# Kernel optimization log

Measured on AMD Instinct MI355X. Metric: run time of the kernel, lower is better.

## Reference

```python
import jax, jax.numpy as jnp
import numpy as np


def setup_inputs() -> dict:
    key = jax.random.key(0)
    k1, k2, k3, k4 = jax.random.split(key, 4)
    batch, T, state_dim, action_dim = 64, 1024, 512, 128
    x0 = jax.random.normal(k1, (batch, state_dim), dtype=jnp.float32)
    us = jax.random.normal(k2, (batch, T, action_dim), dtype=jnp.float32)
    # Scale A so the 1024-step linear recurrence stays bounded (spectral radius < 1)
    A = jax.random.normal(k3, (state_dim, state_dim), dtype=jnp.float32) * (0.9 / np.sqrt(state_dim))
    B = jax.random.normal(k4, (action_dim, state_dim), dtype=jnp.float32) * (1.0 / np.sqrt(action_dim))
    return {"x0": x0, "us": us, "A": A, "B": B}


def reference(x0, us, A, B):
    """Linear SSM rollout: x_{t+1} = x_t @ A + u_t @ B, returns xs [batch, T, state_dim]."""
    us_t = jnp.swapaxes(us, 0, 1)  # [T, batch, action_dim]

    def step(x, u):
        x_next = x @ A + u @ B  # [batch, state_dim]
        return x_next, x_next

    _, xs = jax.lax.scan(step, x0, us_t)  # xs: [T, batch, state_dim]
    return jnp.swapaxes(xs, 0, 1)  # [batch, T, state_dim]
```

## Files before the change

kernel.cpp:

```cpp
#include <hip/hip_runtime.h>


typedef __attribute__((ext_vector_type(8))) short bf16x8;
typedef __attribute__((ext_vector_type(8))) unsigned short ushort8;
typedef __attribute__((ext_vector_type(4))) float f32x4;
typedef unsigned short ushort_t;

#define MFMA16(a, b, c) __builtin_amdgcn_mfma_f32_16x16x32_bf16(a, b, c, 0, 0, 0)

#define OFF_AT  0UL
#define OFF_AU  8912896UL
#define OFF_BT  15204352UL
#define OFF_BU  15335424UL
#define OFF_WT  15466496UL
#define OFF_Z   16515072UL
#define OFF_E1S 41680896UL
#define OFF_E2S 50069504UL

__host__ __device__ __forceinline__ int slot_of(int p) {
    if (p == 0) return 16;
    if (p <= 8) return p - 1;
    return 7 + (p >> 3);
}

__device__ __forceinline__ unsigned short f2bf(float f) {
    union { float f; unsigned u; } v; v.f = f;
    unsigned r = v.u + 0x7FFFu + ((v.u >> 16) & 1u);
    return (unsigned short)(r >> 16);
}

__device__ __forceinline__ int sel4(int4 v, int p) {
    return p == 0 ? v.x : p == 1 ? v.y : p == 2 ? v.z : v.w;
}

typedef __attribute__((address_space(3))) unsigned int as3_u32;
typedef __attribute__((address_space(1))) const unsigned int as1_u32;
__device__ __forceinline__ void gll16(const void* g, void* l) {
    __builtin_amdgcn_global_load_lds((as1_u32*)g, (as3_u32*)l, 16, 0, 0);
}

__global__ __launch_bounds__(256) void prep_kernel(const float* __restrict__ A,
                                                   char* __restrict__ ws) {
    ushort_t* At1 = (ushort_t*)(ws + OFF_AT);
    ushort_t* Au1 = (ushort_t*)(ws + OFF_AU);
    long idx = (long)blockIdx.x * 256 + threadIdx.x;
    if (idx < 262144) {
        Au1[idx] = f2bf(A[idx]);
    } else {
        long gi = idx - 262144;
        int n = (int)(gi >> 9), k = (int)(gi & 511);
        At1[gi] = f2bf(A[(long)k * 512 + n]);
    }
}

__device__ __forceinline__ void pow_tile(char* __restrict__ ws, ushort_t* ldsX,
                                         int d, int m_, int i_, int prod,
                                         int mb, int nb) {
    ushort_t* At = (ushort_t*)(ws + OFF_AT);
    ushort_t* Au = (ushort_t*)(ws + OFF_AU);
    const ushort_t *Xp, *Yp; ushort_t* outp;
    if (prod == 0) { Xp = At + (long)slot_of(m_) * 262144; Yp = Au + (long)slot_of(i_) * 262144; outp = At + (long)slot_of(d) * 262144; }
    else           { Xp = Au + (long)slot_of(i_) * 262144; Yp = At + (long)slot_of(m_) * 262144; outp = Au + (long)slot_of(d) * 262144; }

    int tid = threadIdx.x, w = tid >> 6, lane = tid & 63, q = lane >> 4, r = lane & 15;

    for (int i2 = tid; i2 < 64 * 64; i2 += 256) {
        int row = i2 >> 6, c8 = i2 & 63;
        ushort8 v = *(const ushort8*)(Xp + (long)(mb * 64 + row) * 512 + c8 * 8);
        *(ushort8*)&ldsX[row * 512 + ((c8 ^ (row & 7)) << 3)] = v;
    }
    __syncthreads();

    f32x4 acc[4][2];
    for (int a1 = 0; a1 < 4; a1++) for (int b1 = 0; b1 < 2; b1++) acc[a1][b1] = (f32x4){0.f, 0.f, 0.f, 0.f};

    int n0 = nb * 128 + w * 32;
    for (int kt = 0; kt < 16; kt++) {
        bf16x8 b0 = *(const bf16x8*)(Yp + (long)(n0 + r) * 512 + kt * 32 + q * 8);
        bf16x8 b1 = *(const bf16x8*)(Yp + (long)(n0 + 16 + r) * 512 + kt * 32 + q * 8);
        int g2 = kt * 4 + q;
#pragma unroll
        for (int mi = 0; mi < 4; mi++) {
            int row = mi * 16 + r;
            bf16x8 a = *(bf16x8*)&ldsX[row * 512 + ((g2 ^ (row & 7)) << 3)];
            acc[mi][0] = MFMA16(a, b0, acc[mi][0]);
            acc[mi][1] = MFMA16(a, b1, acc[mi][1]);
        }
    }
    for (int mi = 0; mi < 4; mi++) for (int nj = 0; nj < 2; nj++) {
        int m = mb * 64 + mi * 16 + q * 4, n = n0 + nj * 16 + r;
        for (int v = 0; v < 4; v++) outp[(long)(m + v) * 512 + n] = f2bf(acc[mi][nj][v]);
    }
}

__device__ __forceinline__ void wk_tile(char* __restrict__ ws, ushort_t* ldsX,
                                        int k8, int mb) {
    ushort_t* At = (ushort_t*)(ws + OFF_AT);
    ushort_t* Bu = (ushort_t*)(ws + OFF_BU);
    ushort_t* Bt = (ushort_t*)(ws + OFF_BT);
    ushort_t* Wt = (ushort_t*)(ws + OFF_WT);

    int tid = threadIdx.x, w = tid >> 6, lane = tid & 63, q = lane >> 4, r = lane & 15;

    if (k8 == 7) {
        for (int i2 = tid; i2 < 64 * 32; i2 += 256) {
            int row = i2 >> 5, c4 = i2 & 31;
            ushort4 v = *(const ushort4*)(Bt + (long)(mb * 64 + row) * 128 + c4 * 4);
            *(ushort4*)(Wt + (long)(mb * 64 + row) * 128 + c4 * 4) = v;
        }
        return;
    }

    int p = 7 - k8;
    const ushort_t* Xp = At + (long)slot_of(p) * 262144;
    for (int i2 = tid; i2 < 64 * 64; i2 += 256) {
        int row = i2 >> 6, c8 = i2 & 63;
        ushort8 v = *(const ushort8*)(Xp + (long)(mb * 64 + row) * 512 + c8 * 8);
        *(ushort8*)&ldsX[row * 512 + ((c8 ^ (row & 7)) << 3)] = v;
    }
    __syncthreads();

    f32x4 acc[4][2];
    for (int a1 = 0; a1 < 4; a1++) for (int b1 = 0; b1 < 2; b1++) acc[a1][b1] = (f32x4){0.f, 0.f, 0.f, 0.f};

    int n0 = w * 32;
    for (int kt = 0; kt < 16; kt++) {
        bf16x8 b0 = *(const bf16x8*)(Bu + (long)(n0 + r) * 512 + kt * 32 + q * 8);
        bf16x8 b1 = *(const bf16x8*)(Bu + (long)(n0 + 16 + r) * 512 + kt * 32 + q * 8);
        int g2 = kt * 4 + q;
#pragma unroll
        for (int mi = 0; mi < 4; mi++) {
            int row = mi * 16 + r;
            bf16x8 a = *(bf16x8*)&ldsX[row * 512 + ((g2 ^ (row & 7)) << 3)];
            acc[mi][0] = MFMA16(a, b0, acc[mi][0]);
            acc[mi][1] = MFMA16(a, b1, acc[mi][1]);
        }
    }
    ushort_t* Wp = Wt + (long)p * 65536;
    for (int mi = 0; mi < 4; mi++) for (int nj = 0; nj < 2; nj++) {
        int m = mb * 64 + mi * 16 + q * 4, n = n0 + nj * 16 + r;
        for (int v = 0; v < 4; v++) Wp[(long)(m + v) * 128 + n] = f2bf(acc[mi][nj][v]);
    }
}

__global__ __launch_bounds__(256) void pow_stage(char* __restrict__ ws,
                                                 const float* __restrict__ us,
                                                 const float* __restrict__ x0,
                                                 const float* __restrict__ B,
                                                 int4 dd, int4 mm, int4 ii,
                                                 int dual, int wkbase,
                                                 int ubase, int umode,
                                                 int ustart, int uend) {
    __shared__ ushort_t ldsX[64 * 512];
    int bx = blockIdx.x;

    if (ubase > 0 && bx >= ubase) {
        int tid = threadIdx.x;
        int nthr = (256 - ubase) * 256;
        if (umode == 0) {
            ushort_t* Z = (ushort_t*)(ws + OFF_Z);
            for (long gi = ustart + (long)(bx - ubase) * 256 + tid; gi < uend; gi += nthr) {
                int row = (int)(gi >> 7), g8 = (int)(gi & 127);
                int c = row >> 6, b = row & 63;
                const float* src = us + (long)b * 131072 + c * 1024 + g8 * 8;
                float4 v0 = *(const float4*)src;
                float4 v1 = *(const float4*)(src + 4);
                ushort8 h = { f2bf(v0.x), f2bf(v0.y), f2bf(v0.z), f2bf(v0.w),
                              f2bf(v1.x), f2bf(v1.y), f2bf(v1.z), f2bf(v1.w) };
                *(ushort8*)(Z + (long)row * 1536 + 512 + g8 * 8) = h;
            }
        } else {
            ushort_t* Bt  = (ushort_t*)(ws + OFF_BT);
            ushort_t* Bu  = (ushort_t*)(ws + OFF_BU);
            ushort_t* X0b = (ushort_t*)(ws + OFF_E2S);
            ushort_t* At1 = (ushort_t*)(ws + OFF_AT);
            for (long i = (long)(bx - ubase) * 256 + tid; i < 331776; i += nthr) {
                if (i < 65536) {
                    int kp = (int)(i >> 9), n = (int)(i & 511);
                    ushort_t v = f2bf(B[i]);
                    Bt[(long)n * 128 + kp] = v;
                    Bu[i] = v;
                } else if (i < 69632) {
                    long gi = i - 65536;
                    long e0 = gi * 8;
                    float4 v0 = *(const float4*)(x0 + e0);
                    float4 v1 = *(const float4*)(x0 + e0 + 4);
                    ushort8 h = { f2bf(v0.x), f2bf(v0.y), f2bf(v0.z), f2bf(v0.w),
                                  f2bf(v1.x), f2bf(v1.y), f2bf(v1.z), f2bf(v1.w) };
                    *(ushort8*)(X0b + e0) = h;
                } else {
                    long gi2 = i - 69632;
                    int n = (int)(gi2 >> 9), k2 = (int)(gi2 & 511);
                    At1[(long)16 * 262144 + gi2] = (n == k2) ? (ushort_t)0x3F80 : (ushort_t)0;
                }
            }
        }
        return;
    }
    if (wkbase > 0 && bx >= wkbase) {
        int widx = bx - wkbase;
        wk_tile(ws, ldsX, widx >> 3, widx & 7);
        return;
    }

    int nb = bx & 3, mb = (bx >> 2) & 7;
    int prod, pair;
    if (dual) { prod = (bx >> 5) & 1; pair = bx >> 6; }
    else      { prod = 0;             pair = bx >> 5; }
    int d = sel4(dd, pair), m_ = sel4(mm, pair), i_ = sel4(ii, pair);
    pow_tile(ws, ldsX, d, m_, i_, prod, mb, nb);
}

__global__ __launch_bounds__(256, 4) void e1g(char* __restrict__ ws) {
    __shared__ ushort_t Alds[64 * 64];
    __shared__ ushort_t Blds[128 * 64];
    const ushort_t* Z  = (const ushort_t*)(ws + OFF_Z);
    const ushort_t* Wt = (const ushort_t*)(ws + OFF_WT);
    ushort_t* E1s = (ushort_t*)(ws + OFF_E1S);

    int bx = blockIdx.x;
    int c = bx >> 2, nt = bx & 3;
    int tid = threadIdx.x, w = tid >> 6, lane = tid & 63, q = lane >> 4, r = lane & 15;
    int wr = w >> 1, wc = w & 1;
    int l8 = lane >> 3, srcg = (lane & 7) ^ l8;

    const ushort_t* Xb = Z + (long)c * 64 * 1536 + 512;

    f32x4 acc[2][4];
#pragma unroll
    for (int a1 = 0; a1 < 2; a1++)
#pragma unroll
        for (int b1 = 0; b1 < 4; b1++) acc[a1][b1] = (f32x4){0.f, 0.f, 0.f, 0.f};

    for (int s = 0; s < 16; s++) {
        int k0 = s * 64;
#pragma unroll
        for (int i = 0; i < 2; i++) {
            int row = i * 32 + w * 8 + l8;
            gll16(Xb + (long)row * 1536 + k0 + srcg * 8, &Alds[i * 2048 + w * 512]);
        }
        const ushort_t* Yb = Wt + (long)(7 - (s >> 1)) * 65536 + (s & 1) * 64;
#pragma unroll
        for (int i = 0; i < 4; i++) {
            int row = i * 32 + w * 8 + l8;
            gll16(Yb + (long)(nt * 128 + row) * 128 + srcg * 8, &Blds[i * 2048 + w * 512]);
        }
        __syncthreads();
#pragma unroll
        for (int kt = 0; kt < 2; kt++) {
            int g2 = kt * 4 + q;
            bf16x8 a[2], b[4];
#pragma unroll
            for (int mi = 0; mi < 2; mi++) {
                int row = wr * 32 + mi * 16 + r;
                a[mi] = *(bf16x8*)&Alds[row * 64 + ((g2 ^ (row & 7)) << 3)];
            }
#pragma unroll
            for (int nj = 0; nj < 4; nj++) {
                int row = wc * 64 + nj * 16 + r;
                b[nj] = *(bf16x8*)&Blds[row * 64 + ((g2 ^ (row & 7)) << 3)];
            }
#pragma unroll
            for (int mi = 0; mi < 2; mi++)
#pragma unroll
                for (int nj = 0; nj < 4; nj++)
                    acc[mi][nj] = MFMA16(a[mi], b[nj], acc[mi][nj]);
        }
        __syncthreads();
    }

#pragma unroll
    for (int mi = 0; mi < 2; mi++)
#pragma unroll
        for (int nj = 0; nj < 4; nj++) {
            int m = wr * 32 + mi * 16 + q * 4;
            int n = nt * 128 + wc * 64 + nj * 16 + r;
#pragma unroll
            for (int v = 0; v < 4; v++)
                E1s[(long)c * 32768 + (long)(m + v) * 512 + n] = f2bf(acc[mi][nj][v]);
        }
}

__global__ __launch_bounds__(256, 4) void e2g(char* __restrict__ ws) {
    __shared__ ushort_t Alds[32 * 64];
    __shared__ ushort_t Blds[32 * 64];
    const ushort_t* At  = (const ushort_t*)(ws + OFF_AT);
    const ushort_t* E1s = (const ushort_t*)(ws + OFF_E1S);
    ushort_t* E2s = (ushort_t*)(ws + OFF_E2S);

    int bx = blockIdx.x;
    int g = bx >> 5, mb = (bx >> 4) & 1, ntb = bx & 15;
    int tid = threadIdx.x, w = tid >> 6, lane = tid & 63, q = lane >> 4, r = lane & 15;
    int wr = w >> 1, wc = w & 1;
    int l8 = lane >> 3, srcg = (lane & 7) ^ l8;

    f32x4 acc = (f32x4){0.f, 0.f, 0.f, 0.f};

    for (int s = 0; s < 64; s++) {
        int t = s >> 3, k0 = (s & 7) * 64;
        const ushort_t* Xp = E1s + (long)(8 * g + t) * 32768 + (long)mb * 32 * 512;
        const ushort_t* Yb = At + (long)slot_of(8 * (7 - t)) * 262144;
        {
            int row = w * 8 + l8;
            gll16(Xp + (long)row * 512 + k0 + srcg * 8, &Alds[w * 512]);
            gll16(Yb + (long)(ntb * 32 + row) * 512 + k0 + srcg * 8, &Blds[w * 512]);
        }
        __syncthreads();
#pragma unroll
        for (int kt = 0; kt < 2; kt++) {
            int g2 = kt * 4 + q;
            int arow = wr * 16 + r;
            bf16x8 a = *(bf16x8*)&Alds[arow * 64 + ((g2 ^ (arow & 7)) << 3)];
            int brow = wc * 16 + r;
            bf16x8 b = *(bf16x8*)&Blds[brow * 64 + ((g2 ^ (brow & 7)) << 3)];
            acc = MFMA16(a, b, acc);
        }
        __syncthreads();
    }

    {
        int m = mb * 32 + wr * 16 + q * 4;
        int n = ntb * 32 + wc * 16 + r;
#pragma unroll
        for (int v = 0; v < 4; v++)
            E2s[(long)(1 + g) * 32768 + (long)(m + v) * 512 + n] = f2bf(acc[v]);
    }
}

__global__ __launch_bounds__(256, 4) void s1x(float* __restrict__ dout,
                                              char* __restrict__ ws) {
    __shared__ ushort_t Alds[64 * 64];
    __shared__ ushort_t Blds[128 * 64];
    const ushort_t* At  = (const ushort_t*)(ws + OFF_AT);
    const ushort_t* E1s = (const ushort_t*)(ws + OFF_E1S);
    const ushort_t* E2s = (const ushort_t*)(ws + OFF_E2S);
    ushort_t* Z = (ushort_t*)(ws + OFF_Z);

    int bx = blockIdx.x;
    int t0 = bx >> 2, nt = bx & 3;
    int g, j;
    if (t0 == 128) { g = 16; j = 0; }
    else {
        g = t0 >> 3;
        int jj = t0 & 7;
        j = (g >= 8) ? (7 - jj) : jj;
    }
    int c = g * 8 + j;
    int extra = (j == 0 && g >= 1) ? 1 : 0;
    int nterms = 1 + extra + j;
    int S = nterms * 8;
    int tid = threadIdx.x, w = tid >> 6, lane = tid & 63, q = lane >> 4, r = lane & 15;
    int wr = w >> 1, wc = w & 1;
    int l8 = lane >> 3, srcg = (lane & 7) ^ l8;

    auto xptr = [&](int t) -> const ushort_t* {
        if (t == 0) return E2s + (long)g * 32768;
        if (extra && t == 1) return E2s + (long)(g - 1) * 32768;
        return E1s + (long)(8 * g + t - 1 - extra) * 32768;
    };
    auto yptr = [&](int t) -> const ushort_t* {
        int p = (t == 0) ? 8 * j : ((extra && t == 1) ? 64 : 8 * (j - t + extra));
        return At + (long)slot_of(p) * 262144;
    };

    f32x4 acc[2][4];
#pragma unroll
    for (int a1 = 0; a1 < 2; a1++)
#pragma unroll
        for (int b1 = 0; b1 < 4; b1++) acc[a1][b1] = (f32x4){0.f, 0.f, 0.f, 0.f};

    for (int s = 0; s < S; s++) {
        int t = s >> 3, k0 = (s & 7) * 64;
        const ushort_t* Xp = xptr(t);
        const ushort_t* Yb = yptr(t);
#pragma unroll
        for (int i = 0; i < 2; i++) {
            int row = i * 32 + w * 8 + l8;
            gll16(Xp + (long)row * 512 + k0 + srcg * 8, &Alds[i * 2048 + w * 512]);
        }
#pragma unroll
        for (int i = 0; i < 4; i++) {
            int row = i * 32 + w * 8 + l8;
            gll16(Yb + (long)(nt * 128 + row) * 512 + k0 + srcg * 8, &Blds[i * 2048 + w * 512]);
        }
        __syncthreads();
#pragma unroll
        for (int kt = 0; kt < 2; kt++) {
            int g2 = kt * 4 + q;
            bf16x8 a[2], b[4];
#pragma unroll
            for (int mi = 0; mi < 2; mi++) {
                int row = wr * 32 + mi * 16 + r;
                a[mi] = *(bf16x8*)&Alds[row * 64 + ((g2 ^ (row & 7)) << 3)];
            }
#pragma unroll
            for (int nj = 0; nj < 4; nj++) {
                int row = wc * 64 + nj * 16 + r;
                b[nj] = *(bf16x8*)&Blds[row * 64 + ((g2 ^ (row & 7)) << 3)];
            }
#pragma unroll
            for (int mi = 0; mi < 2; mi++)
#pragma unroll
                for (int nj = 0; nj < 4; nj++)
                    acc[mi][nj] = MFMA16(a[mi], b[nj], acc[mi][nj]);
        }
        __syncthreads();
    }

#pragma unroll
    for (int mi = 0; mi < 2; mi++)
#pragma unroll
        for (int nj = 0; nj < 4; nj++) {
            int m = wr * 32 + mi * 16 + q * 4;
            int n = nt * 128 + wc * 64 + nj * 16 + r;
#pragma unroll
            for (int v = 0; v < 4; v++) {
                float val = acc[mi][nj][v];
                int row = m + v;
                if (c < 128)
                    Z[(long)(c * 64 + row) * 1536 + n] = f2bf(val);
                if (c >= 1)
                    dout[(long)row * 524288 + (long)(8 * c - 1) * 512 + n] = val;
            }
        }
}

__global__ __launch_bounds__(256, 4) void outg(float* __restrict__ dout,
                                               char* __restrict__ ws) {
    __shared__ ushort_t Alds[128 * 64];
    __shared__ ushort_t Blds[128 * 64];
    const ushort_t* Z  = (const ushort_t*)(ws + OFF_Z);
    const ushort_t* At = (const ushort_t*)(ws + OFF_AT);
    const ushort_t* Wt = (const ushort_t*)(ws + OFF_WT);
    ushort_t* M = (ushort_t*)(ws + OFF_E1S);

    int bx = blockIdx.x;
    int nt = bx >> 8;
    int rem = bx & 255;
    int k = 3 - (rem >> 6);
    int mt = rem & 63;
    int tid = threadIdx.x, w = tid >> 6, lane = tid & 63, q = lane >> 4, r = lane & 15;
    int wr = w >> 1, wc = w & 1;
    int l8 = lane >> 3, srcg = (lane & 7) ^ l8;

    const ushort_t* Xb = Z + (long)mt * 128 * 1536;
    const ushort_t* Ya = At + (long)slot_of(k + 1) * 262144;
    int Ks = 8 + 2 * (k + 1);

    f32x4 acc[4][4];
#pragma unroll
    for (int a1 = 0; a1 < 4; a1++)
#pragma unroll
        for (int b1 = 0; b1 < 4; b1++) acc[a1][b1] = (f32x4){0.f, 0.f, 0.f, 0.f};

    for (int s = 0; s < Ks; s++) {
        int k0 = s * 64;
#pragma unroll
        for (int i = 0; i < 4; i++) {
            int row = i * 32 + w * 8 + l8;
            gll16(Xb + (long)row * 1536 + k0 + srcg * 8, &Alds[i * 2048 + w * 512]);
        }
        if (k0 < 512) {
#pragma unroll
            for (int i = 0; i < 4; i++) {
                int row = i * 32 + w * 8 + l8;
                gll16(Ya + (long)(nt * 128 + row) * 512 + k0 + srcg * 8, &Blds[i * 2048 + w * 512]);
            }
        } else {
            int uc = k0 - 512;
            const ushort_t* Yb = Wt + (long)(k - (uc >> 7)) * 65536 + (uc & 127);
#pragma unroll
            for (int i = 0; i < 4; i++) {
                int row = i * 32 + w * 8 + l8;
                gll16(Yb + (long)(nt * 128 + row) * 128 + srcg * 8, &Blds[i * 2048 + w * 512]);
            }
        }
        __syncthreads();
#pragma unroll
        for (int kt = 0; kt < 2; kt++) {
            int g2 = kt * 4 + q;
            bf16x8 a[4], b[4];
#pragma unroll
            for (int mi = 0; mi < 4; mi++) {
                int row = wr * 64 + mi * 16 + r;
                a[mi] = *(bf16x8*)&Alds[row * 64 + ((g2 ^ (row & 7)) << 3)];
            }
#pragma unroll
            for (int nj = 0; nj < 4; nj++) {
                int row = wc * 64 + nj * 16 + r;
                b[nj] = *(bf16x8*)&Blds[row * 64 + ((g2 ^ (row & 7)) << 3)];
            }
#pragma unroll
            for (int mi = 0; mi < 4; mi++)
#pragma unroll
                for (int nj = 0; nj < 4; nj++)
                    acc[mi][nj] = MFMA16(a[mi], b[nj], acc[mi][nj]);
        }
        __syncthreads();
    }

#pragma unroll
    for (int mi = 0; mi < 4; mi++) {
        int m = mt * 128 + wr * 64 + mi * 16 + q * 4;
#pragma unroll
        for (int nj = 0; nj < 4; nj++) {
            int n = nt * 128 + wc * 64 + nj * 16 + r;
#pragma unroll
            for (int v = 0; v < 4; v++) {
                int mm = m + v;
                float val = acc[mi][nj][v];
                dout[(long)(mm & 63) * 524288 + (long)(((mm >> 6) << 3) + k) * 512 + n] = val;
                if (k == 3)
                    M[(long)mm * 512 + n] = f2bf(val);
            }
        }
    }
}

__global__ __launch_bounds__(256, 4) void outg2(float* __restrict__ dout,
                                                char* __restrict__ ws) {
    __shared__ ushort_t Alds[128 * 64];
    __shared__ ushort_t Blds[128 * 64];
    const ushort_t* Z  = (const ushort_t*)(ws + OFF_Z);
    const ushort_t* At = (const ushort_t*)(ws + OFF_AT);
    const ushort_t* Wt = (const ushort_t*)(ws + OFF_WT);
    const ushort_t* M  = (const ushort_t*)(ws + OFF_E1S);

    int bx = blockIdx.x;
    int nt = bx / 192;
    int rem = bx - nt * 192;
    int kp = 2 - (rem >> 6);
    int mt = rem & 63;
    int tid = threadIdx.x, w = tid >> 6, lane = tid & 63, q = lane >> 4, r = lane & 15;
    int wr = w >> 1, wc = w & 1;
    int l8 = lane >> 3, srcg = (lane & 7) ^ l8;

    const ushort_t* Xm = M + (long)mt * 128 * 512;
    const ushort_t* Xu = Z + (long)mt * 128 * 1536 + 1024;
    const ushort_t* Ya = At + (long)slot_of(kp + 1) * 262144;
    int Ks = 8 + 2 * (kp + 1);

    f32x4 acc[4][4];
#pragma unroll
    for (int a1 = 0; a1 < 4; a1++)
#pragma unroll
        for (int b1 = 0; b1 < 4; b1++) acc[a1][b1] = (f32x4){0.f, 0.f, 0.f, 0.f};

    for (int s = 0; s < Ks; s++) {
        int k0 = s * 64;
        if (k0 < 512) {
#pragma unroll
            for (int i = 0; i < 4; i++) {
                int row = i * 32 + w * 8 + l8;
                gll16(Xm + (long)row * 512 + k0 + srcg * 8, &Alds[i * 2048 + w * 512]);
            }
#pragma unroll
            for (int i = 0; i < 4; i++) {
                int row = i * 32 + w * 8 + l8;
                gll16(Ya + (long)(nt * 128 + row) * 512 + k0 + srcg * 8, &Blds[i * 2048 + w * 512]);
            }
        } else {
            int uc = k0 - 512;
#pragma unroll
            for (int i = 0; i < 4; i++) {
                int row = i * 32 + w * 8 + l8;
                gll16(Xu + (long)row * 1536 + uc + srcg * 8, &Alds[i * 2048 + w * 512]);
            }
            const ushort_t* Yb = Wt + (long)(kp - (uc >> 7)) * 65536 + (uc & 127);
#pragma unroll
            for (int i = 0; i < 4; i++) {
                int row = i * 32 + w * 8 + l8;
                gll16(Yb + (long)(nt * 128 + row) * 128 + srcg * 8, &Blds[i * 2048 + w * 512]);
            }
        }
        __syncthreads();
#pragma unroll
        for (int kt = 0; kt < 2; kt++) {
            int g2 = kt * 4 + q;
            bf16x8 a[4], b[4];
#pragma unroll
            for (int mi = 0; mi < 4; mi++) {
                int row = wr * 64 + mi * 16 + r;
                a[mi] = *(bf16x8*)&Alds[row * 64 + ((g2 ^ (row & 7)) << 3)];
            }
#pragma unroll
            for (int nj = 0; nj < 4; nj++) {
                int row = wc * 64 + nj * 16 + r;
                b[nj] = *(bf16x8*)&Blds[row * 64 + ((g2 ^ (row & 7)) << 3)];
            }
#pragma unroll
            for (int mi = 0; mi < 4; mi++)
#pragma unroll
                for (int nj = 0; nj < 4; nj++)
                    acc[mi][nj] = MFMA16(a[mi], b[nj], acc[mi][nj]);
        }
        __syncthreads();
    }

#pragma unroll
    for (int mi = 0; mi < 4; mi++) {
        int m = mt * 128 + wr * 64 + mi * 16 + q * 4;
#pragma unroll
        for (int nj = 0; nj < 4; nj++) {
            int n = nt * 128 + wc * 64 + nj * 16 + r;
#pragma unroll
            for (int v = 0; v < 4; v++) {
                int mm = m + v;
                dout[(long)(mm & 63) * 524288 + (long)(((mm >> 6) << 3) + 4 + kp) * 512 + n] = acc[mi][nj][v];
            }
        }
    }
}

extern "C" void kernel_launch(void* const* d_in, const int* in_sizes, int n_in,
                              void* d_out, int out_size, void* d_ws, size_t ws_size,
                              hipStream_t stream) {
    const float* x0 = (const float*)d_in[0];
    const float* us = (const float*)d_in[1];
    const float* A  = (const float*)d_in[2];
    const float* B  = (const float*)d_in[3];
    float* dout = (float*)d_out;
    char* ws = (char*)d_ws;

    prep_kernel<<<2048, 256, 0, stream>>>(A, ws);

    const int stdual[6]  = {1, 1, 1, 1, 1, 0};
    const int stwk[6]    = {0, 0, 0, 64, 0, 0};
    const int stub[6]    = {64, 128, 0, 128, 128, 128};
    const int stum[6]    = {1, 0, 0, 0, 0, 0};
    const int stus[6]    = {0, 0, 0, 262144, 524288, 786432};
    const int stue[6]    = {0, 262144, 0, 524288, 786432, 1048576};
    const int stpw[6]    = {64, 128, 256, 64, 128, 128};
    const int std_[6][4] = {{2,0,0,0},{3,4,0,0},{5,6,7,8},{16,0,0,0},{24,32,0,0},{40,48,56,64}};
    const int stm[6][4]  = {{1,0,0,0},{2,2,0,0},{4,4,4,4},{8,0,0,0},{16,16,0,0},{32,32,32,32}};
    const int sti[6][4]  = {{1,0,0,0},{1,2,0,0},{1,2,3,4},{8,0,0,0},{8,16,0,0},{8,16,24,32}};
    for (int s = 0; s < 6; s++) {
        int4 dd = {std_[s][0], std_[s][1], std_[s][2], std_[s][3]};
        int4 mm = {stm[s][0], stm[s][1], stm[s][2], stm[s][3]};
        int4 ii = {sti[s][0], sti[s][1], sti[s][2], sti[s][3]};
        int blocks = (stub[s] > 0) ? 256 : stpw[s] + stwk[s];
        pow_stage<<<blocks, 256, 0, stream>>>(ws, us, x0, B, dd, mm, ii,
                                              stdual[s], stwk[s], stub[s],
                                              stum[s], stus[s], stue[s]);
    }

    e1g<<<512, 256, 0, stream>>>(ws);
    e2g<<<512, 256, 0, stream>>>(ws);
    s1x<<<516, 256, 0, stream>>>(dout, ws);
    outg<<<1024, 256, 0, stream>>>(dout, ws);
    outg2<<<768, 256, 0, stream>>>(dout, ws);
}
```

Before: 243.5 us.

## Split s1x into two stages reusing chunk-4 states for later chunk offsets

The s1x stage is split in two. The first kernel computes chunk offsets j=0..4 (plus the final one) as before. A new kernel s1x2 computes offsets j=5..7 starting from the already-computed state at offset 4 (read back from Z), so each needs only j-4+1 terms instead of j+1. This cuts the GEMM work for the high-j offsets, at the cost of an extra kernel launch and a serial dependency between the two launches.

```diff
diff --git a/kernel.cpp b/kernel.cpp
--- a/kernel.cpp
+++ b/kernel.cpp
@@ -339,12 +339,8 @@
     int bx = blockIdx.x;
     int t0 = bx >> 2, nt = bx & 3;
     int g, j;
-    if (t0 == 128) { g = 16; j = 0; }
-    else {
-        g = t0 >> 3;
-        int jj = t0 & 7;
-        j = (g >= 8) ? (7 - jj) : jj;
-    }
+    if (t0 == 80) { g = 16; j = 0; }
+    else { g = t0 / 5; j = t0 - g * 5; }
     int c = g * 8 + j;
     int extra = (j == 0 && g >= 1) ? 1 : 0;
     int nterms = 1 + extra + j;
@@ -421,6 +417,96 @@
                     Z[(long)(c * 64 + row) * 1536 + n] = f2bf(val);
                 if (c >= 1)
                     dout[(long)row * 524288 + (long)(8 * c - 1) * 512 + n] = val;
+            }
+        }
+}
+
+__global__ __launch_bounds__(256, 4) void s1x2(float* __restrict__ dout,
+                                               char* __restrict__ ws) {
+    __shared__ ushort_t Alds[64 * 64];
+    __shared__ ushort_t Blds[128 * 64];
+    const ushort_t* At  = (const ushort_t*)(ws + OFF_AT);
+    const ushort_t* E1s = (const ushort_t*)(ws + OFF_E1S);
+    ushort_t* Z = (ushort_t*)(ws + OFF_Z);
+
+    int bx = blockIdx.x;
+    int t0 = bx >> 2, nt = bx & 3;
+    int g = t0 / 3, jp = t0 - g * 3;
+    int j = 5 + jp;
+    int c = g * 8 + j;
+    int nterms = 1 + (j - 4);
+    int S = nterms * 8;
+    int tid = threadIdx.x, w = tid >> 6, lane = tid & 63, q = lane >> 4, r = lane & 15;
+    int wr = w >> 1, wc = w & 1;
+    int l8 = lane >> 3, srcg = (lane & 7) ^ l8;
+
+    const ushort_t* Tg = Z + (long)(g * 8 + 4) * 64 * 1536;
+
+    f32x4 acc[2][4];
+#pragma unroll
+    for (int a1 = 0; a1 < 2; a1++)
+#pragma unroll
+        for (int b1 = 0; b1 < 4; b1++) acc[a1][b1] = (f32x4){0.f, 0.f, 0.f, 0.f};
+
+    for (int s = 0; s < S; s++) {
+        int t = s >> 3, k0 = (s & 7) * 64;
+        if (t == 0) {
+#pragma unroll
+            for (int i = 0; i < 2; i++) {
+                int row = i * 32 + w * 8 + l8;
+                gll16(Tg + (long)row * 1536 + k0 + srcg * 8, &Alds[i * 2048 + w * 512]);
+            }
+        } else {
+            const ushort_t* Xp = E1s + (long)(8 * g + 3 + t) * 32768;
+#pragma unroll
+            for (int i = 0; i < 2; i++) {
+                int row = i * 32 + w * 8 + l8;
+                gll16(Xp + (long)row * 512 + k0 + srcg * 8, &Alds[i * 2048 + w * 512]);
+            }
+        }
+        int p = (t == 0) ? 8 * (j - 4) : 8 * (j - 4 - t);
+        const ushort_t* Yb = At + (long)slot_of(p) * 262144;
+#pragma unroll
+        for (int i = 0; i < 4; i++) {
+            int row = i * 32 + w * 8 + l8;
+            gll16(Yb + (long)(nt * 128 + row) * 512 + k0 + srcg * 8, &Blds[i * 2048 + w * 512]);
+        }
+        __syncthreads();
+#pragma unroll
+        for (int kt = 0; kt < 2; kt++) {
+            int g2 = kt * 4 + q;
+            bf16x8 a[2], b[4];
+#pragma unroll
+            for (int mi = 0; mi < 2; mi++) {
+                int row = wr * 32 + mi * 16 + r;
+                a[mi] = *(bf16x8*)&Alds[row * 64 + ((g2 ^ (row & 7)) << 3)];
+            }
+#pragma unroll
+            for (int nj = 0; nj < 4; nj++) {
+                int row = wc * 64 + nj * 16 + r;
+                b[nj] = *(bf16x8*)&Blds[row * 64 + ((g2 ^ (row & 7)) << 3)];
+            }
+#pragma unroll
+            for (int mi = 0; mi < 2; mi++)
+#pragma unroll
+                for (int nj = 0; nj < 4; nj++)
+                    acc[mi][nj] = MFMA16(a[mi], b[nj], acc[mi][nj]);
+        }
+        __syncthreads();
+    }
+
+#pragma unroll
+    for (int mi = 0; mi < 2; mi++)
+#pragma unroll
+        for (int nj = 0; nj < 4; nj++) {
+            int m = wr * 32 + mi * 16 + q * 4;
+            int n = nt * 128 + wc * 64 + nj * 16 + r;
+#pragma unroll
+            for (int v = 0; v < 4; v++) {
+                float val = acc[mi][nj][v];
+                int row = m + v;
+                Z[(long)(c * 64 + row) * 1536 + n] = f2bf(val);
+                dout[(long)row * 524288 + (long)(8 * c - 1) * 512 + n] = val;
             }
         }
 }
@@ -646,7 +732,8 @@
 
     e1g<<<512, 256, 0, stream>>>(ws);
     e2g<<<512, 256, 0, stream>>>(ws);
-    s1x<<<516, 256, 0, stream>>>(dout, ws);
+    s1x<<<324, 256, 0, stream>>>(dout, ws);
+    s1x2<<<192, 256, 0, stream>>>(dout, ws);
     outg<<<1024, 256, 0, stream>>>(dout, ws);
     outg2<<<768, 256, 0, stream>>>(dout, ws);
 }
```

Measured after the change: 250.7 us. +2.9%, slower.
